# Performance work log

Measured on AMD Instinct MI355X. Metric: run time of the kernel, lower is better.

## Reference

```python
import jax, jax.numpy as jnp
import numpy as np


def _chamfer(samp_pc, ref_pc):
    """Squared-L2 chamfer: returns (cost_p1_p2 [B,N], cost_p2_p1 [B,M]).

    samp_pc: [B, N, 3], ref_pc: [B, M, 3]
    """
    s2 = jnp.sum(samp_pc * samp_pc, axis=-1)  # [B, N]
    r2 = jnp.sum(ref_pc * ref_pc, axis=-1)    # [B, M]
    cross = jnp.einsum('bnd,bmd->bnm', samp_pc, ref_pc)  # [B, N, M]
    d2 = s2[:, :, None] + r2[:, None, :] - 2.0 * cross   # [B, N, M]
    d2 = jnp.maximum(d2, 0.0)  # numerical floor
    cost_p1_p2 = jnp.min(d2, axis=2)  # [B, N] nearest ref for each samp point
    cost_p2_p1 = jnp.min(d2, axis=1)  # [B, M] nearest samp for each ref point
    return cost_p1_p2, cost_p2_p1


def setup_inputs() -> dict:
    key = jax.random.key(0)
    k1, k2 = jax.random.split(key)
    B, N, M = 16, 2048, 8192
    ref_pc = jax.random.normal(k1, (B, M, 3), dtype=jnp.float32)
    samp_pc = jax.random.normal(k2, (B, N, 3), dtype=jnp.float32)
    return {"ref_pc": ref_pc, "samp_pc": samp_pc}


def reference(ref_pc, samp_pc):
    cost_p1_p2, cost_p2_p1 = _chamfer(samp_pc, ref_pc)
    cd_p = (jnp.sqrt(cost_p1_p2).mean(axis=1) + jnp.sqrt(cost_p2_p1).mean(axis=1)) / 2.0
    cd_t = cost_p1_p2.mean(axis=1) + cost_p2_p1.mean(axis=1)
    return (cd_p, cd_t)
```

## Files before the change

### kernel.cpp

```cpp
#include <hip/hip_runtime.h>
#include <math.h>

#define BB 16
#define NN 2048
#define MM 8192

#define BLK 256
#define R 4
#define G (BLK * R)
#define YS (MM / G)
#define QCH 32
#define ZS (NN / QCH)
#define QPH 16
#define PHASES (QCH / QPH)

typedef float v2f __attribute__((ext_vector_type(2)));

static __device__ __forceinline__ v2f v2_splat(float s) { v2f r; r.x = s; r.y = s; return r; }
static __device__ __forceinline__ v2f v2_fma(v2f a, v2f b, v2f c) {
#if __has_builtin(__builtin_elementwise_fma)
    return __builtin_elementwise_fma(a, b, c);
#else
    v2f r; r.x = fmaf(a.x, b.x, c.x); r.y = fmaf(a.y, b.y, c.y); return r;
#endif
}


__global__ void __launch_bounds__(BLK) prep_kernel(const float* __restrict__ ref,
                                                   const float* __restrict__ samp,
                                                   float4* __restrict__ ref4,
                                                   float4* __restrict__ samp_pk,
                                                   unsigned int* __restrict__ ws2) {
    int i = blockIdx.x * blockDim.x + threadIdx.x;
    const int PM = BB * MM;
    const int PPAIR = BB * NN / 2;
    if (i < PM) {
        float p1 = ref[(size_t)i * 3 + 0], p2 = ref[(size_t)i * 3 + 1], p3 = ref[(size_t)i * 3 + 2];
        float q = fmaf(p1, p1, fmaf(p2, p2, p3 * p3));
        ref4[i] = make_float4(-2.f * p1, -2.f * p2, -2.f * p3, q);
        ws2[i] = 0x7F800000u;
    } else if (i < PM + PPAIR) {
        int k = i - PM;
        const float* s0 = samp + (size_t)k * 6;
        float x0 = s0[0], y0 = s0[1], z0 = s0[2];
        float x1 = s0[3], y1 = s0[4], z1 = s0[5];
        float w0 = fmaf(x0, x0, fmaf(y0, y0, z0 * z0));
        float w1 = fmaf(x1, x1, fmaf(y1, y1, z1 * z1));
        samp_pk[(size_t)k * 2 + 0] = make_float4(x0, x1, y0, y1);
        samp_pk[(size_t)k * 2 + 1] = make_float4(z0, z1, w0, w1);
    }
}

__global__ void __launch_bounds__(BLK, 5) sweep_kernel(const float4* __restrict__ ref4,
                                                       const float4* __restrict__ samp_pk,
                                                       unsigned int* __restrict__ ws2,
                                                       float* __restrict__ ws1p) {
    __shared__ v2f tqbuf[(QPH / 2) * BLK];
    const int b = blockIdx.x;
    const int lane = threadIdx.x & 63;
    const int wv = threadIdx.x >> 6;
    const int refbase = blockIdx.y * G + wv * (64 * R);

    const float4* rp = ref4 + (size_t)b * MM + refbase;
    float px[R], py[R], pz[R], pp[R], mref[R];
#pragma unroll
    for (int r = 0; r < R; ++r) {
        float4 v = rp[r * 64 + lane];
        px[r] = v.x; py[r] = v.y; pz[r] = v.z; pp[r] = v.w;
        mref[r] = INFINITY;
    }

    const int q0 = blockIdx.z * QCH;
    const float4* qt = samp_pk + (size_t)b * NN + q0;
    float* w1 = ws1p + (size_t)blockIdx.y * (BB * NN) + (size_t)b * NN + q0;

    for (int ph = 0; ph < PHASES; ++ph) {
        const float4* qp = qt + ph * QPH;

#pragma unroll 4
        for (int j = 0; j < QPH / 2; ++j) {
            float4 a = qp[2 * j];
            float4 c = qp[2 * j + 1];
            v2f qx; qx.x = a.x; qx.y = a.y;
            v2f qy; qy.x = a.z; qy.y = a.w;
            v2f qz; qz.x = c.x; qz.y = c.y;
            v2f qw; qw.x = c.z; qw.y = c.w;
            v2f t[R];
#pragma unroll
            for (int r = 0; r < R; ++r) {
                v2f s = v2_fma(v2_splat(px[r]), qx, v2_splat(pp[r]));
                s = v2_fma(v2_splat(py[r]), qy, s);
                s = v2_fma(v2_splat(pz[r]), qz, s);
                t[r] = s + qw;
            }
#pragma unroll
            for (int r = 0; r < R; ++r)
                mref[r] = fminf(fminf(mref[r], t[r].x), t[r].y);
            v2f o;
            o.x = fminf(fminf(t[0].x, t[1].x), fminf(t[2].x, t[3].x));
            o.y = fminf(fminf(t[0].y, t[1].y), fminf(t[2].y, t[3].y));
            tqbuf[j * BLK + threadIdx.x] = o;
        }
        __syncthreads();

#pragma unroll
        for (int jj = 0; jj < (QPH / 2) / 4; ++jj) {
            const int jp = wv * ((QPH / 2) / 4) + jj;
            const v2f* s2 = tqbuf + jp * BLK;
            v2f v0 = s2[lane], v1 = s2[lane + 64], v2_ = s2[lane + 128], v3 = s2[lane + 192];
            float m0 = fminf(fminf(v0.x, v1.x), fminf(v2_.x, v3.x));
            float m1 = fminf(fminf(v0.y, v1.y), fminf(v2_.y, v3.y));
#pragma unroll
            for (int s = 32; s > 0; s >>= 1) {
                m0 = fminf(m0, __shfl_xor(m0, s));
                m1 = fminf(m1, __shfl_xor(m1, s));
            }
            if (lane == 0) {
                float2 st; st.x = m0; st.y = m1;
                *(float2*)(w1 + ph * QPH + 2 * jp) = st;
            }
        }
        __syncthreads();
    }

    unsigned int* w2 = ws2 + (size_t)b * MM + refbase;
#pragma unroll
    for (int r = 0; r < R; ++r)
        atomicMin(&w2[r * 64 + lane], __float_as_uint(fmaxf(mref[r], 0.f)));
}

#define BLKR 1024
__global__ void __launch_bounds__(BLKR) reduce_kernel(const float* __restrict__ ws1p,
                                                      const unsigned int* __restrict__ ws2,
                                                      float* __restrict__ out) {
    const int b = blockIdx.x;
    const int tid = threadIdx.x;

    float sd1 = 0.f, sr1 = 0.f;
    for (int i = tid; i < NN; i += BLKR) {
        float m = INFINITY;
#pragma unroll
        for (int y = 0; y < YS; ++y)
            m = fminf(m, ws1p[(size_t)y * (BB * NN) + (size_t)b * NN + i]);
        float v = fmaxf(m, 0.f);
        sd1 += v;
        sr1 += sqrtf(v);
    }
    float sd2 = 0.f, sr2 = 0.f;
    for (int i = tid; i < MM; i += BLKR) {
        float v = __uint_as_float(ws2[(size_t)b * MM + i]);
        sd2 += v;
        sr2 += sqrtf(v);
    }

    __shared__ float4 red[BLKR];
    red[tid] = make_float4(sd1, sr1, sd2, sr2);
    __syncthreads();
    for (int s = BLKR / 2; s > 0; s >>= 1) {
        if (tid < s) {
            red[tid].x += red[tid + s].x;
            red[tid].y += red[tid + s].y;
            red[tid].z += red[tid + s].z;
            red[tid].w += red[tid + s].w;
        }
        __syncthreads();
    }
    if (tid == 0) {
        float4 r = red[0];
        out[b]      = (r.y * (1.0f / NN) + r.w * (1.0f / MM)) * 0.5f;
        out[BB + b] = r.x * (1.0f / NN) + r.z * (1.0f / MM);
    }
}

extern "C" void kernel_launch(void* const* d_in, const int* in_sizes, int n_in,
                              void* d_out, int out_size, void* d_ws, size_t ws_size,
                              hipStream_t stream) {
    const float* ref  = (const float*)d_in[0];
    const float* samp = (const float*)d_in[1];
    float* out = (float*)d_out;

    float4* ref4    = (float4*)d_ws;
    float4* samp_pk = ref4 + (size_t)BB * MM;
    unsigned int* ws2 = (unsigned int*)(samp_pk + (size_t)BB * NN);
    float* ws1p = (float*)(ws2 + (size_t)BB * MM);

    const int P = BB * MM + BB * NN / 2;
    prep_kernel<<<(P + BLK - 1) / BLK, BLK, 0, stream>>>(ref, samp, ref4, samp_pk, ws2);

    dim3 gs(BB, YS, ZS);
    sweep_kernel<<<gs, BLK, 0, stream>>>(ref4, samp_pk, ws2, ws1p);

    reduce_kernel<<<BB, BLKR, 0, stream>>>(ws1p, ws2, out);
}
```

Before: 100.0 us.

## Fuse preprocessing into sweep, double ref tile, use atomicMin for row minima

Removes the separate prep kernel. Each sweep block now computes its reference-point norms and packed query tile, placed in shared memory, from the raw inputs. The per-thread reference count rises from 4 to 8, halving the Y split. Per-Y partial row minima are replaced by atomicMin into a single buffer that a memset initialises, which makes the reduce kernel simpler and has it use wave shuffles. The trade-offs are more register pressure, redundant norm computation per block, and extra atomics.

```diff
diff --git a/kernel.cpp b/kernel.cpp
--- a/kernel.cpp
+++ b/kernel.cpp
@@ -6,7 +6,7 @@
 #define MM 8192
 
 #define BLK 256
-#define R 4
+#define R 8
 #define G (BLK * R)
 #define YS (MM / G)
 #define QCH 32
@@ -26,61 +26,50 @@
 }
 
 
-__global__ void __launch_bounds__(BLK) prep_kernel(const float* __restrict__ ref,
-                                                   const float* __restrict__ samp,
-                                                   float4* __restrict__ ref4,
-                                                   float4* __restrict__ samp_pk,
-                                                   unsigned int* __restrict__ ws2) {
-    int i = blockIdx.x * blockDim.x + threadIdx.x;
-    const int PM = BB * MM;
-    const int PPAIR = BB * NN / 2;
-    if (i < PM) {
-        float p1 = ref[(size_t)i * 3 + 0], p2 = ref[(size_t)i * 3 + 1], p3 = ref[(size_t)i * 3 + 2];
-        float q = fmaf(p1, p1, fmaf(p2, p2, p3 * p3));
-        ref4[i] = make_float4(-2.f * p1, -2.f * p2, -2.f * p3, q);
-        ws2[i] = 0x7F800000u;
-    } else if (i < PM + PPAIR) {
-        int k = i - PM;
-        const float* s0 = samp + (size_t)k * 6;
+__global__ void __launch_bounds__(BLK, 5) sweep_kernel(const float* __restrict__ ref,
+                                                       const float* __restrict__ samp,
+                                                       unsigned int* __restrict__ ws2,
+                                                       unsigned int* __restrict__ ws1) {
+    __shared__ v2f tqbuf[(QPH / 2) * BLK];
+    __shared__ float4 qbuf[QCH];
+
+    const int b = blockIdx.x;
+    const int lane = threadIdx.x & 63;
+    const int wv = threadIdx.x >> 6;
+    const int refbase = blockIdx.y * G + wv * (64 * R);
+    const int q0 = blockIdx.z * QCH;
+
+    if (threadIdx.x < QCH / 2) {
+        const int k = threadIdx.x;
+        const float* s0 = samp + ((size_t)b * NN + q0 + 2 * k) * 3;
         float x0 = s0[0], y0 = s0[1], z0 = s0[2];
         float x1 = s0[3], y1 = s0[4], z1 = s0[5];
         float w0 = fmaf(x0, x0, fmaf(y0, y0, z0 * z0));
         float w1 = fmaf(x1, x1, fmaf(y1, y1, z1 * z1));
-        samp_pk[(size_t)k * 2 + 0] = make_float4(x0, x1, y0, y1);
-        samp_pk[(size_t)k * 2 + 1] = make_float4(z0, z1, w0, w1);
+        qbuf[2 * k]     = make_float4(x0, x1, y0, y1);
+        qbuf[2 * k + 1] = make_float4(z0, z1, w0, w1);
     }
-}
 
-__global__ void __launch_bounds__(BLK, 5) sweep_kernel(const float4* __restrict__ ref4,
-                                                       const float4* __restrict__ samp_pk,
-                                                       unsigned int* __restrict__ ws2,
-                                                       float* __restrict__ ws1p) {
-    __shared__ v2f tqbuf[(QPH / 2) * BLK];
-    const int b = blockIdx.x;
-    const int lane = threadIdx.x & 63;
-    const int wv = threadIdx.x >> 6;
-    const int refbase = blockIdx.y * G + wv * (64 * R);
-
-    const float4* rp = ref4 + (size_t)b * MM + refbase;
+    const float* rp = ref + ((size_t)b * MM + refbase) * 3;
     float px[R], py[R], pz[R], pp[R], mref[R];
 #pragma unroll
     for (int r = 0; r < R; ++r) {
-        float4 v = rp[r * 64 + lane];
-        px[r] = v.x; py[r] = v.y; pz[r] = v.z; pp[r] = v.w;
+        const float* pq = rp + (size_t)(r * 64 + lane) * 3;
+        float p1 = pq[0], p2 = pq[1], p3 = pq[2];
+        pp[r] = fmaf(p1, p1, fmaf(p2, p2, p3 * p3));
+        px[r] = -2.f * p1; py[r] = -2.f * p2; pz[r] = -2.f * p3;
         mref[r] = INFINITY;
     }
+    __syncthreads();
 
-    const int q0 = blockIdx.z * QCH;
-    const float4* qt = samp_pk + (size_t)b * NN + q0;
-    float* w1 = ws1p + (size_t)blockIdx.y * (BB * NN) + (size_t)b * NN + q0;
+    unsigned int* w1 = ws1 + (size_t)b * NN + q0;
 
     for (int ph = 0; ph < PHASES; ++ph) {
-        const float4* qp = qt + ph * QPH;
-
-#pragma unroll 4
+#pragma unroll 2
         for (int j = 0; j < QPH / 2; ++j) {
-            float4 a = qp[2 * j];
-            float4 c = qp[2 * j + 1];
+            const int jp = ph * (QPH / 2) + j;
+            float4 a = qbuf[2 * jp];
+            float4 c = qbuf[2 * jp + 1];
             v2f qx; qx.x = a.x; qx.y = a.y;
             v2f qy; qy.x = a.z; qy.y = a.w;
             v2f qz; qz.x = c.x; qz.y = c.y;
@@ -97,8 +86,14 @@
             for (int r = 0; r < R; ++r)
                 mref[r] = fminf(fminf(mref[r], t[r].x), t[r].y);
             v2f o;
-            o.x = fminf(fminf(t[0].x, t[1].x), fminf(t[2].x, t[3].x));
-            o.y = fminf(fminf(t[0].y, t[1].y), fminf(t[2].y, t[3].y));
+            {
+                float a0 = fminf(t[0].x, t[1].x), a1 = fminf(t[2].x, t[3].x);
+                float a2 = fminf(t[4].x, t[5].x), a3 = fminf(t[6].x, t[7].x);
+                o.x = fminf(fminf(a0, a1), fminf(a2, a3));
+                float b0 = fminf(t[0].y, t[1].y), b1 = fminf(t[2].y, t[3].y);
+                float b2 = fminf(t[4].y, t[5].y), b3 = fminf(t[6].y, t[7].y);
+                o.y = fminf(fminf(b0, b1), fminf(b2, b3));
+            }
             tqbuf[j * BLK + threadIdx.x] = o;
         }
         __syncthreads();
@@ -116,8 +111,8 @@
                 m1 = fminf(m1, __shfl_xor(m1, s));
             }
             if (lane == 0) {
-                float2 st; st.x = m0; st.y = m1;
-                *(float2*)(w1 + ph * QPH + 2 * jp) = st;
+                atomicMin(&w1[ph * QPH + 2 * jp],     __float_as_uint(fmaxf(m0, 0.f)));
+                atomicMin(&w1[ph * QPH + 2 * jp + 1], __float_as_uint(fmaxf(m1, 0.f)));
             }
         }
         __syncthreads();
@@ -130,45 +125,47 @@
 }
 
 #define BLKR 1024
-__global__ void __launch_bounds__(BLKR) reduce_kernel(const float* __restrict__ ws1p,
+__global__ void __launch_bounds__(BLKR) reduce_kernel(const unsigned int* __restrict__ ws1,
                                                       const unsigned int* __restrict__ ws2,
                                                       float* __restrict__ out) {
     const int b = blockIdx.x;
     const int tid = threadIdx.x;
+    const int lane = tid & 63;
+    const int wv = tid >> 6;
 
-    float sd1 = 0.f, sr1 = 0.f;
+    float sd1 = 0.f, sr1 = 0.f, sd2 = 0.f, sr2 = 0.f;
+#pragma unroll
     for (int i = tid; i < NN; i += BLKR) {
-        float m = INFINITY;
-#pragma unroll
-        for (int y = 0; y < YS; ++y)
-            m = fminf(m, ws1p[(size_t)y * (BB * NN) + (size_t)b * NN + i]);
-        float v = fmaxf(m, 0.f);
+        float v = __uint_as_float(ws1[(size_t)b * NN + i]);
         sd1 += v;
         sr1 += sqrtf(v);
     }
-    float sd2 = 0.f, sr2 = 0.f;
+#pragma unroll
     for (int i = tid; i < MM; i += BLKR) {
         float v = __uint_as_float(ws2[(size_t)b * MM + i]);
         sd2 += v;
         sr2 += sqrtf(v);
     }
+#pragma unroll
+    for (int s = 32; s > 0; s >>= 1) {
+        sd1 += __shfl_xor(sd1, s);
+        sr1 += __shfl_xor(sr1, s);
+        sd2 += __shfl_xor(sd2, s);
+        sr2 += __shfl_xor(sr2, s);
+    }
 
-    __shared__ float4 red[BLKR];
-    red[tid] = make_float4(sd1, sr1, sd2, sr2);
+    __shared__ float4 red[BLKR / 64];
+    if (lane == 0) red[wv] = make_float4(sd1, sr1, sd2, sr2);
     __syncthreads();
-    for (int s = BLKR / 2; s > 0; s >>= 1) {
-        if (tid < s) {
-            red[tid].x += red[tid + s].x;
-            red[tid].y += red[tid + s].y;
-            red[tid].z += red[tid + s].z;
-            red[tid].w += red[tid + s].w;
+    if (tid == 0) {
+        float4 acc = red[0];
+#pragma unroll
+        for (int w = 1; w < BLKR / 64; ++w) {
+            acc.x += red[w].x; acc.y += red[w].y;
+            acc.z += red[w].z; acc.w += red[w].w;
         }
-        __syncthreads();
-    }
-    if (tid == 0) {
-        float4 r = red[0];
-        out[b]      = (r.y * (1.0f / NN) + r.w * (1.0f / MM)) * 0.5f;
-        out[BB + b] = r.x * (1.0f / NN) + r.z * (1.0f / MM);
+        out[b]      = (acc.y * (1.0f / NN) + acc.w * (1.0f / MM)) * 0.5f;
+        out[BB + b] = acc.x * (1.0f / NN) + acc.z * (1.0f / MM);
     }
 }
 
@@ -179,16 +176,13 @@
     const float* samp = (const float*)d_in[1];
     float* out = (float*)d_out;
 
-    float4* ref4    = (float4*)d_ws;
-    float4* samp_pk = ref4 + (size_t)BB * MM;
-    unsigned int* ws2 = (unsigned int*)(samp_pk + (size_t)BB * NN);
-    float* ws1p = (float*)(ws2 + (size_t)BB * MM);
+    unsigned int* ws2 = (unsigned int*)d_ws;
+    unsigned int* ws1 = ws2 + (size_t)BB * MM;
 
-    const int P = BB * MM + BB * NN / 2;
-    prep_kernel<<<(P + BLK - 1) / BLK, BLK, 0, stream>>>(ref, samp, ref4, samp_pk, ws2);
+    hipMemsetAsync(d_ws, 0x7F, ((size_t)BB * MM + (size_t)BB * NN) * sizeof(unsigned int), stream);
 
     dim3 gs(BB, YS, ZS);
-    sweep_kernel<<<gs, BLK, 0, stream>>>(ref4, samp_pk, ws2, ws1p);
+    sweep_kernel<<<gs, BLK, 0, stream>>>(ref, samp, ws2, ws1);
 
-    reduce_kernel<<<BB, BLKR, 0, stream>>>(ws1p, ws2, out);
+    reduce_kernel<<<BB, BLKR, 0, stream>>>(ws1, ws2, out);
 }
```

Result: slower. 244.5 us (+144.5%).
